# Kernel optimization log

Measured on AMD Instinct MI355X. Metric: run time of the kernel, lower is better.

Reference implementation:

```python
import jax, jax.numpy as jnp
import numpy as np

N = 40000; E = 500000; IN = 128; ED = 16; HID = 64; HEADS = 4; OUT = 256; B = 128
NEG = 0.2  # GATv2 leaky_relu negative slope


def _add_self_loops(edge_index, edge_attr, n):
    # PyG add_self_loops with fill_value='mean': loop attr = mean of incoming edge attrs per node
    dst = edge_index[1]
    s = jax.ops.segment_sum(edge_attr, dst, num_segments=n)
    c = jax.ops.segment_sum(jnp.ones((edge_attr.shape[0],), edge_attr.dtype), dst, num_segments=n)
    loop_attr = s / jnp.maximum(c, 1.0)[:, None]
    loops = jnp.arange(n, dtype=edge_index.dtype)
    ei = jnp.concatenate([edge_index, jnp.stack([loops, loops])], axis=1)
    ea = jnp.concatenate([edge_attr, loop_attr], axis=0)
    return ei, ea


def _seg_softmax(logits, seg, n):
    m = jax.ops.segment_max(logits, seg, num_segments=n)
    m = jnp.where(jnp.isfinite(m), m, 0.0)  # guard empty segments
    e = jnp.exp(logits - m[seg])
    z = jax.ops.segment_sum(e, seg, num_segments=n)
    return e / (z[seg] + 1e-16)


def _gatv2(x, src, dst, ea, Wl, bl, Wr, br, We, att, bias, heads, oc, concat):
    n = x.shape[0]
    xl = (x @ Wl + bl).reshape(n, heads, oc)  # lin_l (source/message transform)
    xr = (x @ Wr + br).reshape(n, heads, oc)  # lin_r (target transform)
    ef = (ea @ We).reshape(-1, heads, oc)     # lin_edge (no bias)
    s = jax.nn.leaky_relu(xl[src] + xr[dst] + ef, NEG)  # [Etot,H,C]
    alpha = _seg_softmax(jnp.einsum('ehc,hc->eh', s, att), dst, n)  # scatter-softmax over dst
    out = jax.ops.segment_sum(xl[src] * alpha[..., None], dst, num_segments=n)  # [N,H,C]
    out = out.reshape(n, heads * oc) if concat else out.mean(axis=1)
    return out + bias


def setup_inputs():
    ks = jax.random.split(jax.random.key(0), 32)
    W = lambda i, shp: jax.random.normal(ks[i], shp, jnp.float32) * 0.05
    z = lambda d: jnp.zeros((d,), jnp.float32)
    H = HEADS * HID
    return dict(
        x=jax.random.normal(ks[0], (N, IN), jnp.float32),
        edge_index=jax.random.randint(ks[1], (2, E), 0, N),
        edge_attr=jax.random.normal(ks[2], (E, ED), jnp.float32),
        batch=jnp.sort(jax.random.randint(ks[3], (N,), 0, B)),
        batch_size=B,
        c1_Wl=W(4, (IN, H)), c1_bl=z(H), c1_Wr=W(5, (IN, H)), c1_br=z(H), c1_We=W(6, (ED, H)), c1_att=W(7, (HEADS, HID)), c1_bias=z(H),
        c2_Wl=W(8, (H, H)), c2_bl=z(H), c2_Wr=W(9, (H, H)), c2_br=z(H), c2_We=W(10, (ED, H)), c2_att=W(11, (HEADS, HID)), c2_bias=z(H),
        c3_Wl=W(12, (H, OUT)), c3_bl=z(OUT), c3_Wr=W(13, (H, OUT)), c3_br=z(OUT), c3_We=W(14, (ED, OUT)), c3_att=W(15, (1, OUT)), c3_bias=z(OUT),
        gate_W1=W(16, (OUT, 128)), gate_b1=z(128), gate_W2=W(17, (128, 1)), gate_b2=z(1),
        reg_W1=W(18, (OUT, 128)), reg_b1=z(128), reg_W2=W(19, (128, 2)), reg_b2=z(2),
    )


def reference(x, edge_index, edge_attr, batch, batch_size,
              c1_Wl, c1_bl, c1_Wr, c1_br, c1_We, c1_att, c1_bias,
              c2_Wl, c2_bl, c2_Wr, c2_br, c2_We, c2_att, c2_bias,
              c3_Wl, c3_bl, c3_Wr, c3_br, c3_We, c3_att, c3_bias,
              gate_W1, gate_b1, gate_W2, gate_b2,
              reg_W1, reg_b1, reg_W2, reg_b2):
    # task_type='homo_lumo' path; dropout disabled (inference)
    ei, ea = _add_self_loops(edge_index, edge_attr, N)
    src, dst = ei[0], ei[1]
    h = jax.nn.relu(_gatv2(x, src, dst, ea, c1_Wl, c1_bl, c1_Wr, c1_br, c1_We, c1_att, c1_bias, HEADS, HID, True))
    h = jax.nn.relu(_gatv2(h, src, dst, ea, c2_Wl, c2_bl, c2_Wr, c2_br, c2_We, c2_att, c2_bias, HEADS, HID, True))
    h = _gatv2(h, src, dst, ea, c3_Wl, c3_bl, c3_Wr, c3_br, c3_We, c3_att, c3_bias, 1, OUT, True)
    # AttentionalAggregation pooling
    gate = jax.nn.relu(h @ gate_W1 + gate_b1) @ gate_W2 + gate_b2  # [N,1]
    a = _seg_softmax(gate[:, 0], batch, batch_size)
    g = jax.ops.segment_sum(h * a[:, None], batch, num_segments=batch_size)  # [B,OUT]
    return jax.nn.relu(g @ reg_W1 + reg_b1) @ reg_W2 + reg_b2  # [B,2]
```

## Files before the change

kernel.cpp:

```cpp
#include <hip/hip_runtime.h>
#include <math.h>

constexpr int N_NODES = 40000;
constexpr int N_EDGES = 500000;
constexpr int ETOT    = N_EDGES + N_NODES;
constexpr int IN_DIM  = 128;
constexpr int ED_DIM  = 16;
constexpr int FEAT    = 256;
constexpr int BATCH   = 128;
constexpr float NEG   = 0.2f;
constexpr int NCHUNK  = (N_NODES + 255) / 256;

typedef __bf16 bf16x8 __attribute__((ext_vector_type(8)));
typedef float  f32x4  __attribute__((ext_vector_type(4)));

__global__ __launch_bounds__(256) void k_deg(const int* __restrict__ dst, int* __restrict__ deg)
{
    int e = blockIdx.x * 256 + threadIdx.x;
    if (e >= ETOT) return;
    int v = e < N_EDGES ? dst[e] : e - N_EDGES;
    atomicAdd(&deg[v], 1);
}

__global__ __launch_bounds__(256) void k_scan1(const int* __restrict__ deg, int* __restrict__ bsum)
{
    __shared__ int s[256];
    int t = threadIdx.x;
    int idx = blockIdx.x * 256 + t;
    s[t] = idx < N_NODES ? deg[idx] : 0;
    __syncthreads();
    for (int st = 128; st; st >>= 1) { if (t < st) s[t] += s[t + st]; __syncthreads(); }
    if (t == 0) bsum[blockIdx.x] = s[0];
}

__global__ __launch_bounds__(256) void k_scan2(const int* __restrict__ bsum,
    int* __restrict__ boff, int* __restrict__ rowptr)
{
    __shared__ int s[256];
    int t = threadIdx.x;
    int v = t < NCHUNK ? bsum[t] : 0;
    s[t] = v;
    __syncthreads();
    for (int off = 1; off < 256; off <<= 1) {
        int x = (t >= off) ? s[t - off] : 0;
        __syncthreads();
        s[t] += x;
        __syncthreads();
    }
    if (t < NCHUNK) boff[t] = s[t] - v;
    if (t == 0) rowptr[N_NODES] = ETOT;
}

__global__ __launch_bounds__(256) void k_scan3(const int* __restrict__ deg,
    const int* __restrict__ boff, int* __restrict__ rowptr)
{
    __shared__ int s[256];
    int t = threadIdx.x;
    int idx = blockIdx.x * 256 + t;
    int v = idx < N_NODES ? deg[idx] : 0;
    s[t] = v;
    __syncthreads();
    for (int off = 1; off < 256; off <<= 1) {
        int x = (t >= off) ? s[t - off] : 0;
        __syncthreads();
        s[t] += x;
        __syncthreads();
    }
    if (idx < N_NODES) rowptr[idx] = boff[blockIdx.x] + s[t] - v;
}

__global__ __launch_bounds__(256) void k_fill(const int* __restrict__ srcA, const int* __restrict__ dst,
    const int* __restrict__ rowptr, int* __restrict__ fill, int2* __restrict__ elist2)
{
    int e = blockIdx.x * 256 + threadIdx.x;
    if (e >= ETOT) return;
    int v = e < N_EDGES ? dst[e]  : e - N_EDGES;
    int s = e < N_EDGES ? srcA[e] : e - N_EDGES;
    int pos = rowptr[v] + atomicAdd(&fill[v], 1);
    elist2[pos] = make_int2(s, e);
}

__global__ __launch_bounds__(256) void k_loop_csr(const int2* __restrict__ elist2,
    const int* __restrict__ rowptr, const float* __restrict__ ea, float* __restrict__ loop_attr)
{
    int t = blockIdx.x * 256 + threadIdx.x;
    if (t >= N_NODES * ED_DIM) return;
    int n = t >> 4, d = t & 15;
    int p0 = rowptr[n], p1 = rowptr[n + 1];
    float s = 0.f; int c = 0;
    for (int p = p0; p < p1; ++p) {
        int e = elist2[p].y;
        if (e < N_EDGES) { s += ea[(size_t)e * ED_DIM + d]; ++c; }
    }
    loop_attr[t] = s / (float)(c > 0 ? c : 1);
}

__device__ __forceinline__ void bsplit(float x, unsigned short& h, unsigned short& l)
{
    unsigned u = __float_as_uint(x);
    unsigned r = (u + 0x7FFFu + ((u >> 16) & 1u)) >> 16;
    h = (unsigned short)r;
    float rem = x - __uint_as_float(r << 16);
    unsigned u2 = __float_as_uint(rem);
    l = (unsigned short)((u2 + 0x7FFFu + ((u2 >> 16) & 1u)) >> 16);
}

__global__ __launch_bounds__(256) void k_cvt(const float* __restrict__ X,
    unsigned short* __restrict__ Xh, unsigned short* __restrict__ Xl, int n4)
{
    int i = blockIdx.x * 256 + threadIdx.x;
    if (i >= n4) return;
    float4 v = ((const float4*)X)[i];
    ushort4 h, l;
    bsplit(v.x, h.x, l.x);
    bsplit(v.y, h.y, l.y);
    bsplit(v.z, h.z, l.z);
    bsplit(v.w, h.w, l.w);
    ((ushort4*)Xh)[i] = h;
    ((ushort4*)Xl)[i] = l;
}

__global__ __launch_bounds__(256) void k_cvtT(const float* __restrict__ W,
    unsigned short* __restrict__ WhT, unsigned short* __restrict__ WlT, int K, int N)
{
    int i = blockIdx.x * 256 + threadIdx.x;
    if (i >= K * N) return;
    int k = i / N, n = i - k * N;
    unsigned short h, l;
    bsplit(W[i], h, l);
    WhT[(size_t)n * K + k] = h;
    WlT[(size_t)n * K + k] = l;
}

__global__ __launch_bounds__(256) void k_mgemm(
    const unsigned short* __restrict__ Ah, const unsigned short* __restrict__ Al,
    const unsigned short* __restrict__ BhT, const unsigned short* __restrict__ BlT,
    const float* __restrict__ bias, float* __restrict__ C,
    int M, int N, int K, int act)
{
    __shared__ uint4 sAh[512], sAl[512], sBh[512], sBl[512];

    int t = threadIdx.x;
    int bm = blockIdx.x * 128, bn = blockIdx.y * 128;
    int lane = t & 63;
    int w = t >> 6;
    int mh = w >> 1, nh = w & 1;

    int sT = t >> 6, sq = (t >> 4) & 3, slm = t & 15;
    int am0 = bm + sT * 16 + slm;        am0 = am0 < M ? am0 : M - 1;
    int am1 = bm + (sT + 4) * 16 + slm;  am1 = am1 < M ? am1 : M - 1;
    int bn0 = bn + sT * 16 + slm;
    int bn1 = bn + (sT + 4) * 16 + slm;
    size_t aoff0 = (size_t)am0 * K + sq * 8;
    size_t aoff1 = (size_t)am1 * K + sq * 8;
    size_t boff0 = (size_t)bn0 * K + sq * 8;
    size_t boff1 = (size_t)bn1 * K + sq * 8;

    f32x4 acc[4][4] = {};

    uint4 rAh0 = *(const uint4*)(Ah + aoff0),  rAh1 = *(const uint4*)(Ah + aoff1);
    uint4 rAl0 = *(const uint4*)(Al + aoff0),  rAl1 = *(const uint4*)(Al + aoff1);
    uint4 rBh0 = *(const uint4*)(BhT + boff0), rBh1 = *(const uint4*)(BhT + boff1);
    uint4 rBl0 = *(const uint4*)(BlT + boff0), rBl1 = *(const uint4*)(BlT + boff1);

    int nk = K >> 5;
    for (int ks = 0; ks < nk; ++ks) {
        sAh[t] = rAh0; sAh[t + 256] = rAh1;
        sAl[t] = rAl0; sAl[t + 256] = rAl1;
        sBh[t] = rBh0; sBh[t + 256] = rBh1;
        sBl[t] = rBl0; sBl[t + 256] = rBl1;
        __syncthreads();
        if (ks + 1 < nk) {
            int k8 = (ks + 1) << 5;
            rAh0 = *(const uint4*)(Ah + aoff0 + k8);  rAh1 = *(const uint4*)(Ah + aoff1 + k8);
            rAl0 = *(const uint4*)(Al + aoff0 + k8);  rAl1 = *(const uint4*)(Al + aoff1 + k8);
            rBh0 = *(const uint4*)(BhT + boff0 + k8); rBh1 = *(const uint4*)(BhT + boff1 + k8);
            rBl0 = *(const uint4*)(BlT + boff0 + k8); rBl1 = *(const uint4*)(BlT + boff1 + k8);
        }
        bf16x8 fah[4], fal[4], fbh[4], fbl[4];
        #pragma unroll
        for (int mt = 0; mt < 4; ++mt) {
            fah[mt] = __builtin_bit_cast(bf16x8, sAh[(mh * 4 + mt) * 64 + lane]);
            fal[mt] = __builtin_bit_cast(bf16x8, sAl[(mh * 4 + mt) * 64 + lane]);
        }
        #pragma unroll
        for (int nt = 0; nt < 4; ++nt) {
            fbh[nt] = __builtin_bit_cast(bf16x8, sBh[(nh * 4 + nt) * 64 + lane]);
            fbl[nt] = __builtin_bit_cast(bf16x8, sBl[(nh * 4 + nt) * 64 + lane]);
        }
        #pragma unroll
        for (int mt = 0; mt < 4; ++mt)
            #pragma unroll
            for (int nt = 0; nt < 4; ++nt) {
                acc[mt][nt] = __builtin_amdgcn_mfma_f32_16x16x32_bf16(fah[mt], fbh[nt], acc[mt][nt], 0, 0, 0);
                acc[mt][nt] = __builtin_amdgcn_mfma_f32_16x16x32_bf16(fah[mt], fbl[nt], acc[mt][nt], 0, 0, 0);
                acc[mt][nt] = __builtin_amdgcn_mfma_f32_16x16x32_bf16(fal[mt], fbh[nt], acc[mt][nt], 0, 0, 0);
            }
        __syncthreads();
    }

    int q = lane >> 4, lm = lane & 15;
    #pragma unroll
    for (int nt = 0; nt < 4; ++nt) {
        int col = bn + nh * 64 + nt * 16 + lm;
        float bb = bias[col];
        #pragma unroll
        for (int mt = 0; mt < 4; ++mt) {
            #pragma unroll
            for (int i = 0; i < 4; ++i) {
                int row = bm + mh * 64 + mt * 16 + q * 4 + i;
                if (row < M) {
                    float o = acc[mt][nt][i] + bb;
                    if (act) o = fmaxf(o, 0.f);
                    C[(size_t)row * N + col] = o;
                }
            }
        }
    }
}

static void launch_mgemm(const unsigned short* Ah, const unsigned short* Al,
                         const unsigned short* BhT, const unsigned short* BlT,
                         const float* bias, float* C, int M, int N, int K, int act,
                         hipStream_t stream)
{
    dim3 grid((M + 127) / 128, N / 128);
    k_mgemm<<<grid, 256, 0, stream>>>(Ah, Al, BhT, BlT, bias, C, M, N, K, act);
}

#define XELOAD(s) do {                                                                \
    int src_ = __builtin_amdgcn_readfirstlane(eS[s].x);                               \
    int e_   = __builtin_amdgcn_readfirstlane(eS[s].y);                               \
    const float4* eb4_ = reinterpret_cast<const float4*>(                             \
        (e_ < N_EDGES) ? ea + (size_t)e_ * ED_DIM                                     \
                       : loop_attr + (size_t)src_ * ED_DIM);                          \
    evS[s][0] = eb4_[0]; evS[s][1] = eb4_[1];                                         \
    evS[s][2] = eb4_[2]; evS[s][3] = eb4_[3];                                         \
    xlvS[s] = *(const float4*)(xl + (size_t)src_ * FEAT + base);                      \
} while (0)

#define COMPUTE(s) do {                                                               \
    float ef0_ = 0.f, ef1_ = 0.f, ef2_ = 0.f, ef3_ = 0.f;                             \
    const float* ed_ = (const float*)evS[s];                                          \
    _Pragma("unroll")                                                                 \
    for (int d_ = 0; d_ < ED_DIM; ++d_) {                                             \
        float a_ = ed_[d_];                                                           \
        ef0_ = fmaf(a_, weR[d_].x, ef0_); ef1_ = fmaf(a_, weR[d_].y, ef1_);           \
        ef2_ = fmaf(a_, weR[d_].z, ef2_); ef3_ = fmaf(a_, weR[d_].w, ef3_);           \
    }                                                                                 \
    float s0_ = xlvS[s].x + xrv.x + ef0_;                                             \
    float s1_ = xlvS[s].y + xrv.y + ef1_;                                             \
    float s2_ = xlvS[s].z + xrv.z + ef2_;                                             \
    float s3_ = xlvS[s].w + xrv.w + ef3_;                                             \
    s0_ = fmaxf(s0_, 0.f) + NEG * fminf(s0_, 0.f);                                    \
    s1_ = fmaxf(s1_, 0.f) + NEG * fminf(s1_, 0.f);                                    \
    s2_ = fmaxf(s2_, 0.f) + NEG * fminf(s2_, 0.f);                                    \
    s3_ = fmaxf(s3_, 0.f) + NEG * fminf(s3_, 0.f);                                    \
    float l_ = fmaf(s0_, attR.x, fmaf(s1_, attR.y, fmaf(s2_, attR.z, s3_ * attR.w))); \
    l_ += __shfl_xor(l_, 1, 64);                                                      \
    l_ += __shfl_xor(l_, 2, 64);                                                      \
    l_ += __shfl_xor(l_, 4, 64);                                                      \
    l_ += __shfl_xor(l_, 8, 64);                                                      \
    if (H == 1) { l_ += __shfl_xor(l_, 16, 64); l_ += __shfl_xor(l_, 32, 64); }       \
    float nm_ = fmaxf(m, l_);                                                         \
    float sc_ = __expf(m - nm_);                                                      \
    float w_  = __expf(l_ - nm_);                                                     \
    z = fmaf(z, sc_, w_);                                                             \
    m = nm_;                                                                          \
    acc.x = fmaf(acc.x, sc_, w_ * xlvS[s].x);                                         \
    acc.y = fmaf(acc.y, sc_, w_ * xlvS[s].y);                                         \
    acc.z = fmaf(acc.z, sc_, w_ * xlvS[s].z);                                         \
    acc.w = fmaf(acc.w, sc_, w_ * xlvS[s].w);                                         \
} while (0)

template <int H, int RELU>
__global__ __launch_bounds__(256, 4) void k_gat(
    const float* __restrict__ xl, const float* __restrict__ xr,
    const float* __restrict__ ea, const float* __restrict__ loop_attr,
    const int2* __restrict__ elist2, const int* __restrict__ rowptr,
    const float* __restrict__ We, const float* __restrict__ att,
    const float* __restrict__ bias, float* __restrict__ out)
{
    int t = threadIdx.x;
    int lane = t & 63;
    int n = __builtin_amdgcn_readfirstlane(blockIdx.x * 4 + (t >> 6));
    int base = lane * 4;

    float4 weR[ED_DIM];
    #pragma unroll
    for (int d = 0; d < ED_DIM; ++d)
        weR[d] = *(const float4*)(We + d * FEAT + base);

    float4 attR = *(const float4*)(att + base);
    float4 xrv  = *(const float4*)(xr + (size_t)n * FEAT + base);

    float m = -INFINITY, z = 0.f;
    float4 acc = {0.f, 0.f, 0.f, 0.f};

    int p0 = rowptr[n], p1 = rowptr[n + 1];
    int pe = p1 - 1;

    int2   eS[2];
    float4 evS[2][4];
    float4 xlvS[2];

    eS[0] = elist2[p0];
    { int pc = p0 + 1 > pe ? pe : p0 + 1; eS[1] = elist2[pc]; }
    XELOAD(0);

    int p = p0;
    while (true) {
        XELOAD(1);
        { int pn = p + 2 > pe ? pe : p + 2; eS[0] = elist2[pn]; }
        COMPUTE(0);
        if (++p >= p1) break;
        XELOAD(0);
        { int pn = p + 2 > pe ? pe : p + 2; eS[1] = elist2[pn]; }
        COMPUTE(1);
        if (++p >= p1) break;
    }

    float inv = 1.0f / (z + 1e-16f);
    float4 bs = *(const float4*)(bias + base);
    float4 o;
    o.x = fmaf(acc.x, inv, bs.x);
    o.y = fmaf(acc.y, inv, bs.y);
    o.z = fmaf(acc.z, inv, bs.z);
    o.w = fmaf(acc.w, inv, bs.w);
    if (RELU) {
        o.x = fmaxf(o.x, 0.f); o.y = fmaxf(o.y, 0.f);
        o.z = fmaxf(o.z, 0.f); o.w = fmaxf(o.w, 0.f);
    }
    *(float4*)(out + (size_t)n * FEAT + base) = o;
}

__global__ __launch_bounds__(256) void k_gate_score(const float* __restrict__ ghid,
    const float* __restrict__ W2, const float* __restrict__ b2, float* __restrict__ gate)
{
    int lane = threadIdx.x & 63;
    int n = blockIdx.x * 4 + (threadIdx.x >> 6);
    float v = ghid[(size_t)n * 128 + lane] * W2[lane] + ghid[(size_t)n * 128 + lane + 64] * W2[lane + 64];
    #pragma unroll
    for (int off = 32; off > 0; off >>= 1) v += __shfl_xor(v, off, 64);
    if (lane == 0) gate[n] = v + b2[0];
}

__device__ __forceinline__ int lbound(const int* a, int n, int v)
{
    int lo = 0, hi = n;
    while (lo < hi) { int mid = (lo + hi) >> 1; if (a[mid] < v) lo = mid + 1; else hi = mid; }
    return lo;
}

__global__ __launch_bounds__(256) void k_pool(const float* __restrict__ gate,
    const float* __restrict__ h, const int* __restrict__ batch, float* __restrict__ g)
{
    int b = blockIdx.x;
    int t = threadIdx.x;
    __shared__ float red[256];
    int start = lbound(batch, N_NODES, b);
    int end   = lbound(batch, N_NODES, b + 1);

    float mx = -INFINITY;
    for (int n = start + t; n < end; n += 256) mx = fmaxf(mx, gate[n]);
    red[t] = mx; __syncthreads();
    for (int s = 128; s; s >>= 1) { if (t < s) red[t] = fmaxf(red[t], red[t + s]); __syncthreads(); }
    float m = red[0];
    __syncthreads();

    float zs = 0.f;
    for (int n = start + t; n < end; n += 256) zs += __expf(gate[n] - m);
    red[t] = zs; __syncthreads();
    for (int s = 128; s; s >>= 1) { if (t < s) red[t] += red[t + s]; __syncthreads(); }
    float z = red[0];

    float gs = 0.f;
    for (int n = start; n < end; ++n) gs += __expf(gate[n] - m) * h[(size_t)n * FEAT + t];
    g[b * FEAT + t] = gs / (z + 1e-16f);
}

__global__ __launch_bounds__(128) void k_reg(const float* __restrict__ g,
    const float* __restrict__ W1, const float* __restrict__ b1,
    const float* __restrict__ W2, const float* __restrict__ b2, float* __restrict__ out)
{
    int b = blockIdx.x, t = threadIdx.x;
    __shared__ float sg[FEAT];
    sg[t] = g[b * FEAT + t];
    sg[t + 128] = g[b * FEAT + t + 128];
    __syncthreads();
    float hv = b1[t];
    for (int k = 0; k < FEAT; ++k) hv += sg[k] * W1[k * 128 + t];
    hv = fmaxf(hv, 0.f);
    __shared__ float p0s[128], p1s[128];
    p0s[t] = hv * W2[t * 2 + 0];
    p1s[t] = hv * W2[t * 2 + 1];
    __syncthreads();
    for (int s = 64; s; s >>= 1) {
        if (t < s) { p0s[t] += p0s[t + s]; p1s[t] += p1s[t + s]; }
        __syncthreads();
    }
    if (t == 0) { out[b * 2 + 0] = p0s[0] + b2[0]; out[b * 2 + 1] = p1s[0] + b2[1]; }
}

extern "C" void kernel_launch(void* const* d_in, const int* in_sizes, int n_in,
                              void* d_out, int out_size, void* d_ws, size_t ws_size,
                              hipStream_t stream)
{
    const float* x       = (const float*)d_in[0];
    const int*   ei      = (const int*)d_in[1];
    const float* ea      = (const float*)d_in[2];
    const int*   batch   = (const int*)d_in[3];
    const float* c1_Wl   = (const float*)d_in[5];
    const float* c1_bl   = (const float*)d_in[6];
    const float* c1_Wr   = (const float*)d_in[7];
    const float* c1_br   = (const float*)d_in[8];
    const float* c1_We   = (const float*)d_in[9];
    const float* c1_att  = (const float*)d_in[10];
    const float* c1_bias = (const float*)d_in[11];
    const float* c2_Wl   = (const float*)d_in[12];
    const float* c2_bl   = (const float*)d_in[13];
    const float* c2_Wr   = (const float*)d_in[14];
    const float* c2_br   = (const float*)d_in[15];
    const float* c2_We   = (const float*)d_in[16];
    const float* c2_att  = (const float*)d_in[17];
    const float* c2_bias = (const float*)d_in[18];
    const float* c3_Wl   = (const float*)d_in[19];
    const float* c3_bl   = (const float*)d_in[20];
    const float* c3_Wr   = (const float*)d_in[21];
    const float* c3_br   = (const float*)d_in[22];
    const float* c3_We   = (const float*)d_in[23];
    const float* c3_att  = (const float*)d_in[24];
    const float* c3_bias = (const float*)d_in[25];
    const float* gate_W1 = (const float*)d_in[26];
    const float* gate_b1 = (const float*)d_in[27];
    const float* gate_W2 = (const float*)d_in[28];
    const float* gate_b2 = (const float*)d_in[29];
    const float* reg_W1  = (const float*)d_in[30];
    const float* reg_b1  = (const float*)d_in[31];
    const float* reg_W2  = (const float*)d_in[32];
    const float* reg_b2  = (const float*)d_in[33];

    const int* srcArr = ei;
    const int* dstArr = ei + N_EDGES;

    float* ws = (float*)d_ws;
    size_t off = 0;
    auto alloc = [&](size_t nf) { float* p = ws + off; off += (nf + 63) & ~(size_t)63; return p; };
    float* xl        = alloc((size_t)N_NODES * FEAT);
    float* xr        = alloc((size_t)N_NODES * FEAT);
    float* h         = alloc((size_t)N_NODES * FEAT);
    float* loop_attr = alloc((size_t)N_NODES * ED_DIM);
    float* gpool     = alloc((size_t)BATCH * FEAT);
    unsigned short* Ah = (unsigned short*)alloc((size_t)N_NODES * FEAT / 2);
    unsigned short* Al = (unsigned short*)alloc((size_t)N_NODES * FEAT / 2);
    unsigned short* wlT_h = (unsigned short*)alloc(FEAT * FEAT / 2);
    unsigned short* wlT_l = (unsigned short*)alloc(FEAT * FEAT / 2);
    unsigned short* wrT_h = (unsigned short*)alloc(FEAT * FEAT / 2);
    unsigned short* wrT_l = (unsigned short*)alloc(FEAT * FEAT / 2);
    int* ibase  = (int*)(ws + off);
    int* deg    = ibase;
    int* fill   = ibase + N_NODES;
    int* rowptr = ibase + 2 * N_NODES;
    int* bsum   = ibase + 3 * N_NODES + 64;
    int* boff   = bsum + 256;
    int2* elist2 = (int2*)(boff + 256);

    float* ghid = xl;
    float* gate = xr;

    hipMemsetAsync(deg, 0, (size_t)2 * N_NODES * sizeof(int), stream);

    k_deg<<<(ETOT + 255) / 256, 256, 0, stream>>>(dstArr, deg);
    k_scan1<<<NCHUNK, 256, 0, stream>>>(deg, bsum);
    k_scan2<<<1, 256, 0, stream>>>(bsum, boff, rowptr);
    k_scan3<<<NCHUNK, 256, 0, stream>>>(deg, boff, rowptr);
    k_fill<<<(ETOT + 255) / 256, 256, 0, stream>>>(srcArr, dstArr, rowptr, fill, elist2);
    k_loop_csr<<<(N_NODES * ED_DIM + 255) / 256, 256, 0, stream>>>(elist2, rowptr, ea, loop_attr);

    {
        int n4 = N_NODES * IN_DIM / 4;
        k_cvt<<<(n4 + 255) / 256, 256, 0, stream>>>(x, Ah, Al, n4);
        k_cvtT<<<(IN_DIM * FEAT + 255) / 256, 256, 0, stream>>>(c1_Wl, wlT_h, wlT_l, IN_DIM, FEAT);
        k_cvtT<<<(IN_DIM * FEAT + 255) / 256, 256, 0, stream>>>(c1_Wr, wrT_h, wrT_l, IN_DIM, FEAT);
        launch_mgemm(Ah, Al, wlT_h, wlT_l, c1_bl, xl, N_NODES, FEAT, IN_DIM, 0, stream);
        launch_mgemm(Ah, Al, wrT_h, wrT_l, c1_br, xr, N_NODES, FEAT, IN_DIM, 0, stream);
    }
    k_gat<4, 1><<<N_NODES / 4, 256, 0, stream>>>(xl, xr, ea, loop_attr, elist2, rowptr,
                                                 c1_We, c1_att, c1_bias, h);
    {
        int n4 = N_NODES * FEAT / 4;
        k_cvt<<<(n4 + 255) / 256, 256, 0, stream>>>(h, Ah, Al, n4);
        k_cvtT<<<(FEAT * FEAT + 255) / 256, 256, 0, stream>>>(c2_Wl, wlT_h, wlT_l, FEAT, FEAT);
        k_cvtT<<<(FEAT * FEAT + 255) / 256, 256, 0, stream>>>(c2_Wr, wrT_h, wrT_l, FEAT, FEAT);
        launch_mgemm(Ah, Al, wlT_h, wlT_l, c2_bl, xl, N_NODES, FEAT, FEAT, 0, stream);
        launch_mgemm(Ah, Al, wrT_h, wrT_l, c2_br, xr, N_NODES, FEAT, FEAT, 0, stream);
    }
    k_gat<4, 1><<<N_NODES / 4, 256, 0, stream>>>(xl, xr, ea, loop_attr, elist2, rowptr,
                                                 c2_We, c2_att, c2_bias, h);
    {
        int n4 = N_NODES * FEAT / 4;
        k_cvt<<<(n4 + 255) / 256, 256, 0, stream>>>(h, Ah, Al, n4);
        k_cvtT<<<(FEAT * FEAT + 255) / 256, 256, 0, stream>>>(c3_Wl, wlT_h, wlT_l, FEAT, FEAT);
        k_cvtT<<<(FEAT * FEAT + 255) / 256, 256, 0, stream>>>(c3_Wr, wrT_h, wrT_l, FEAT, FEAT);
        launch_mgemm(Ah, Al, wlT_h, wlT_l, c3_bl, xl, N_NODES, FEAT, FEAT, 0, stream);
        launch_mgemm(Ah, Al, wrT_h, wrT_l, c3_br, xr, N_NODES, FEAT, FEAT, 0, stream);
    }
    k_gat<1, 0><<<N_NODES / 4, 256, 0, stream>>>(xl, xr, ea, loop_attr, elist2, rowptr,
                                                 c3_We, c3_att, c3_bias, h);

    {
        int n4 = N_NODES * FEAT / 4;
        k_cvt<<<(n4 + 255) / 256, 256, 0, stream>>>(h, Ah, Al, n4);
        k_cvtT<<<(FEAT * 128 + 255) / 256, 256, 0, stream>>>(gate_W1, wlT_h, wlT_l, FEAT, 128);
        launch_mgemm(Ah, Al, wlT_h, wlT_l, gate_b1, ghid, N_NODES, 128, FEAT, 1, stream);
    }
    k_gate_score<<<N_NODES / 4, 256, 0, stream>>>(ghid, gate_W2, gate_b2, gate);
    k_pool<<<BATCH, 256, 0, stream>>>(gate, h, batch, gpool);
    k_reg<<<BATCH, 128, 0, stream>>>(gpool, reg_W1, reg_b1, reg_W2, reg_b2, (float*)d_out);
}
```

Measured before the change: 1.122 ms.

## Fuse bf16 split into GAT epilogue and load GEMM fragments directly from global

The GAT kernel now writes its output directly as bf16 hi/lo split arrays (and fp32 only for the last layer), removing three separate k_cvt conversion passes over the node features. The GEMM drops its shared-memory staging and register double-buffering and reads MFMA fragments straight from global memory each k-step. That removes LDS traffic and barriers but loses the prefetch overlap and relies on cache for reuse across waves.

```diff
diff --git a/kernel.cpp b/kernel.cpp
--- a/kernel.cpp
+++ b/kernel.cpp
@@ -138,55 +138,36 @@
     const float* __restrict__ bias, float* __restrict__ C,
     int M, int N, int K, int act)
 {
-    __shared__ uint4 sAh[512], sAl[512], sBh[512], sBl[512];
-
     int t = threadIdx.x;
-    int bm = blockIdx.x * 128, bn = blockIdx.y * 128;
     int lane = t & 63;
     int w = t >> 6;
     int mh = w >> 1, nh = w & 1;
-
-    int sT = t >> 6, sq = (t >> 4) & 3, slm = t & 15;
-    int am0 = bm + sT * 16 + slm;        am0 = am0 < M ? am0 : M - 1;
-    int am1 = bm + (sT + 4) * 16 + slm;  am1 = am1 < M ? am1 : M - 1;
-    int bn0 = bn + sT * 16 + slm;
-    int bn1 = bn + (sT + 4) * 16 + slm;
-    size_t aoff0 = (size_t)am0 * K + sq * 8;
-    size_t aoff1 = (size_t)am1 * K + sq * 8;
-    size_t boff0 = (size_t)bn0 * K + sq * 8;
-    size_t boff1 = (size_t)bn1 * K + sq * 8;
+    int bm = blockIdx.x * 128, bn = blockIdx.y * 128;
+    int q = lane >> 4, lm = lane & 15;
+
+    size_t aoff[4], boff[4];
+    #pragma unroll
+    for (int mt = 0; mt < 4; ++mt) {
+        int r = bm + mh * 64 + mt * 16 + lm;
+        r = r < M ? r : M - 1;
+        aoff[mt] = (size_t)r * K + q * 8;
+    }
+    #pragma unroll
+    for (int nt = 0; nt < 4; ++nt) {
+        int c = bn + nh * 64 + nt * 16 + lm;
+        boff[nt] = (size_t)c * K + q * 8;
+    }
 
     f32x4 acc[4][4] = {};
 
-    uint4 rAh0 = *(const uint4*)(Ah + aoff0),  rAh1 = *(const uint4*)(Ah + aoff1);
-    uint4 rAl0 = *(const uint4*)(Al + aoff0),  rAl1 = *(const uint4*)(Al + aoff1);
-    uint4 rBh0 = *(const uint4*)(BhT + boff0), rBh1 = *(const uint4*)(BhT + boff1);
-    uint4 rBl0 = *(const uint4*)(BlT + boff0), rBl1 = *(const uint4*)(BlT + boff1);
-
-    int nk = K >> 5;
-    for (int ks = 0; ks < nk; ++ks) {
-        sAh[t] = rAh0; sAh[t + 256] = rAh1;
-        sAl[t] = rAl0; sAl[t + 256] = rAl1;
-        sBh[t] = rBh0; sBh[t + 256] = rBh1;
-        sBl[t] = rBl0; sBl[t + 256] = rBl1;
-        __syncthreads();
-        if (ks + 1 < nk) {
-            int k8 = (ks + 1) << 5;
-            rAh0 = *(const uint4*)(Ah + aoff0 + k8);  rAh1 = *(const uint4*)(Ah + aoff1 + k8);
-            rAl0 = *(const uint4*)(Al + aoff0 + k8);  rAl1 = *(const uint4*)(Al + aoff1 + k8);
-            rBh0 = *(const uint4*)(BhT + boff0 + k8); rBh1 = *(const uint4*)(BhT + boff1 + k8);
-            rBl0 = *(const uint4*)(BlT + boff0 + k8); rBl1 = *(const uint4*)(BlT + boff1 + k8);
-        }
+    for (int k0 = 0; k0 < K; k0 += 32) {
         bf16x8 fah[4], fal[4], fbh[4], fbl[4];
         #pragma unroll
-        for (int mt = 0; mt < 4; ++mt) {
-            fah[mt] = __builtin_bit_cast(bf16x8, sAh[(mh * 4 + mt) * 64 + lane]);
-            fal[mt] = __builtin_bit_cast(bf16x8, sAl[(mh * 4 + mt) * 64 + lane]);
-        }
-        #pragma unroll
-        for (int nt = 0; nt < 4; ++nt) {
-            fbh[nt] = __builtin_bit_cast(bf16x8, sBh[(nh * 4 + nt) * 64 + lane]);
-            fbl[nt] = __builtin_bit_cast(bf16x8, sBl[(nh * 4 + nt) * 64 + lane]);
+        for (int i = 0; i < 4; ++i) {
+            fah[i] = __builtin_bit_cast(bf16x8, *(const uint4*)(Ah  + aoff[i] + k0));
+            fal[i] = __builtin_bit_cast(bf16x8, *(const uint4*)(Al  + aoff[i] + k0));
+            fbh[i] = __builtin_bit_cast(bf16x8, *(const uint4*)(BhT + boff[i] + k0));
+            fbl[i] = __builtin_bit_cast(bf16x8, *(const uint4*)(BlT + boff[i] + k0));
         }
         #pragma unroll
         for (int mt = 0; mt < 4; ++mt)
@@ -196,10 +177,8 @@
                 acc[mt][nt] = __builtin_amdgcn_mfma_f32_16x16x32_bf16(fah[mt], fbl[nt], acc[mt][nt], 0, 0, 0);
                 acc[mt][nt] = __builtin_amdgcn_mfma_f32_16x16x32_bf16(fal[mt], fbh[nt], acc[mt][nt], 0, 0, 0);
             }
-        __syncthreads();
-    }
-
-    int q = lane >> 4, lm = lane & 15;
+    }
+
     #pragma unroll
     for (int nt = 0; nt < 4; ++nt) {
         int col = bn + nh * 64 + nt * 16 + lm;
@@ -273,13 +252,14 @@
     acc.w = fmaf(acc.w, sc_, w_ * xlvS[s].w);                                         \
 } while (0)
 
-template <int H, int RELU>
+template <int H, int RELU, int OUTMODE>
 __global__ __launch_bounds__(256, 4) void k_gat(
     const float* __restrict__ xl, const float* __restrict__ xr,
     const float* __restrict__ ea, const float* __restrict__ loop_attr,
     const int2* __restrict__ elist2, const int* __restrict__ rowptr,
     const float* __restrict__ We, const float* __restrict__ att,
-    const float* __restrict__ bias, float* __restrict__ out)
+    const float* __restrict__ bias, float* __restrict__ out,
+    unsigned short* __restrict__ outH, unsigned short* __restrict__ outL)
 {
     int t = threadIdx.x;
     int lane = t & 63;
@@ -331,7 +311,15 @@
         o.x = fmaxf(o.x, 0.f); o.y = fmaxf(o.y, 0.f);
         o.z = fmaxf(o.z, 0.f); o.w = fmaxf(o.w, 0.f);
     }
-    *(float4*)(out + (size_t)n * FEAT + base) = o;
+    if (OUTMODE == 2)
+        *(float4*)(out + (size_t)n * FEAT + base) = o;
+    ushort4 oh, ol;
+    bsplit(o.x, oh.x, ol.x);
+    bsplit(o.y, oh.y, ol.y);
+    bsplit(o.z, oh.z, ol.z);
+    bsplit(o.w, oh.w, ol.w);
+    *(ushort4*)(outH + (size_t)n * FEAT + base) = oh;
+    *(ushort4*)(outL + (size_t)n * FEAT + base) = ol;
 }
 
 __global__ __launch_bounds__(256) void k_gate_score(const float* __restrict__ ghid,
@@ -485,32 +473,26 @@
         launch_mgemm(Ah, Al, wlT_h, wlT_l, c1_bl, xl, N_NODES, FEAT, IN_DIM, 0, stream);
         launch_mgemm(Ah, Al, wrT_h, wrT_l, c1_br, xr, N_NODES, FEAT, IN_DIM, 0, stream);
     }
-    k_gat<4, 1><<<N_NODES / 4, 256, 0, stream>>>(xl, xr, ea, loop_attr, elist2, rowptr,
-                                                 c1_We, c1_att, c1_bias, h);
+    k_gat<4, 1, 1><<<N_NODES / 4, 256, 0, stream>>>(xl, xr, ea, loop_attr, elist2, rowptr,
+                                                    c1_We, c1_att, c1_bias, h, Ah, Al);
     {
-        int n4 = N_NODES * FEAT / 4;
-        k_cvt<<<(n4 + 255) / 256, 256, 0, stream>>>(h, Ah, Al, n4);
         k_cvtT<<<(FEAT * FEAT + 255) / 256, 256, 0, stream>>>(c2_Wl, wlT_h, wlT_l, FEAT, FEAT);
         k_cvtT<<<(FEAT * FEAT + 255) / 256, 256, 0, stream>>>(c2_Wr, wrT_h, wrT_l, FEAT, FEAT);
         launch_mgemm(Ah, Al, wlT_h, wlT_l, c2_bl, xl, N_NODES, FEAT, FEAT, 0, stream);
         launch_mgemm(Ah, Al, wrT_h, wrT_l, c2_br, xr, N_NODES, FEAT, FEAT, 0, stream);
     }
-    k_gat<4, 1><<<N_NODES / 4, 256, 0, stream>>>(xl, xr, ea, loop_attr, elist2, rowptr,
-                                                 c2_We, c2_att, c2_bias, h);
+    k_gat<4, 1, 1><<<N_NODES / 4, 256, 0, stream>>>(xl, xr, ea, loop_attr, elist2, rowptr,
+                                                    c2_We, c2_att, c2_bias, h, Ah, Al);
     {
-        int n4 = N_NODES * FEAT / 4;
-        k_cvt<<<(n4 + 255) / 256, 256, 0, stream>>>(h, Ah, Al, n4);
         k_cvtT<<<(FEAT * FEAT + 255) / 256, 256, 0, stream>>>(c3_Wl, wlT_h, wlT_l, FEAT, FEAT);
         k_cvtT<<<(FEAT * FEAT + 255) / 256, 256, 0, stream>>>(c3_Wr, wrT_h, wrT_l, FEAT, FEAT);
         launch_mgemm(Ah, Al, wlT_h, wlT_l, c3_bl, xl, N_NODES, FEAT, FEAT, 0, stream);
         launch_mgemm(Ah, Al, wrT_h, wrT_l, c3_br, xr, N_NODES, FEAT, FEAT, 0, stream);
     }
-    k_gat<1, 0><<<N_NODES / 4, 256, 0, stream>>>(xl, xr, ea, loop_attr, elist2, rowptr,
-                                                 c3_We, c3_att, c3_bias, h);
+    k_gat<1, 0, 2><<<N_NODES / 4, 256, 0, stream>>>(xl, xr, ea, loop_attr, elist2, rowptr,
+                                                    c3_We, c3_att, c3_bias, h, Ah, Al);
 
     {
-        int n4 = N_NODES * FEAT / 4;
-        k_cvt<<<(n4 + 255) / 256, 256, 0, stream>>>(h, Ah, Al, n4);
         k_cvtT<<<(FEAT * 128 + 255) / 256, 256, 0, stream>>>(gate_W1, wlT_h, wlT_l, FEAT, 128);
         launch_mgemm(Ah, Al, wlT_h, wlT_l, gate_b1, ghid, N_NODES, 128, FEAT, 1, stream);
     }
```

After: 1.237 ms. +10.3%, slower.
